# Performance work log

Hardware: AMD Instinct MI355X
Metric: run time of the kernel (lower is better)

The kernel has to match this reference:

```python
import jax, jax.numpy as jnp
import numpy as np

D_MODEL = 1024
NUM_HEADS = 16
D_FF = 4096
EPS = 1e-5


def _linear(x, w, b):
    # torch nn.Linear: y = x @ W^T + b, W is [out, in]
    return jnp.einsum('bld,od->blo', x, w) + b


def _layer_norm(x, g, b):
    mu = jnp.mean(x, axis=-1, keepdims=True)
    var = jnp.mean(jnp.square(x - mu), axis=-1, keepdims=True)
    return (x - mu) / jnp.sqrt(var + EPS) * g + b


def _mha(q, k, v, wq, bq, wk, bk, wv, bv, wo, bo, mask, num_heads):
    B, Lq, D = q.shape
    hd = D // num_heads
    Q = _linear(q, wq, bq).reshape(B, Lq, num_heads, hd).transpose(0, 2, 1, 3)
    K = _linear(k, wk, bk).reshape(B, -1, num_heads, hd).transpose(0, 2, 1, 3)
    V = _linear(v, wv, bv).reshape(B, -1, num_heads, hd).transpose(0, 2, 1, 3)
    scale = jnp.sqrt(jnp.asarray(hd, dtype=q.dtype))
    energy = jnp.einsum('bhqd,bhkd->bhqk', Q, K) / scale  # [B,H,Lq,Lk]
    energy = jnp.where(mask, energy, jnp.asarray(-1e10, dtype=q.dtype))
    attn = jax.nn.softmax(energy, axis=-1)
    x = jnp.einsum('bhqk,bhkd->bhqd', attn, V)
    x = x.transpose(0, 2, 1, 3).reshape(B, Lq, D)
    return _linear(x, wo, bo), attn


def setup_inputs() -> dict:
    key = jax.random.key(0)
    ks = iter(jax.random.split(key, 40))
    B, T, S, D, F = 4, 1024, 1024, D_MODEL, D_FF
    inp = {
        'tgt': jax.random.normal(next(ks), (B, T, D), dtype=jnp.float32),
        'enc_src': jax.random.normal(next(ks), (B, S, D), dtype=jnp.float32),
        'tgt_mask': jnp.tril(jnp.ones((1, 1, T, T), dtype=bool)),
        'src_mask': jnp.ones((1, 1, 1, S), dtype=bool),
    }
    def lin(kk, o, i):
        return jax.random.normal(kk, (o, i), dtype=jnp.float32) * 0.02
    for pfx in ('sa', 'ca'):  # self-attn and cross-attn params
        for nm in ('q', 'k', 'v', 'o'):
            inp[f'{pfx}_w{nm}'] = lin(next(ks), D, D)
            inp[f'{pfx}_b{nm}'] = jnp.zeros((D,), dtype=jnp.float32)
    inp['ff_w1'] = lin(next(ks), F, D)
    inp['ff_b1'] = jnp.zeros((F,), dtype=jnp.float32)
    inp['ff_w2'] = lin(next(ks), D, F)
    inp['ff_b2'] = jnp.zeros((D,), dtype=jnp.float32)
    for i in (1, 2, 3):
        inp[f'ln{i}_g'] = jnp.ones((D,), dtype=jnp.float32)
        inp[f'ln{i}_b'] = jnp.zeros((D,), dtype=jnp.float32)
    return inp


def reference(tgt, enc_src, tgt_mask, src_mask,
              sa_wq, sa_bq, sa_wk, sa_bk, sa_wv, sa_bv, sa_wo, sa_bo,
              ca_wq, ca_bq, ca_wk, ca_bk, ca_wv, ca_bv, ca_wo, ca_bo,
              ff_w1, ff_b1, ff_w2, ff_b2,
              ln1_g, ln1_b, ln2_g, ln2_b, ln3_g, ln3_b):
    # dropout in eval mode (identity)
    _t, _ = _mha(tgt, tgt, tgt, sa_wq, sa_bq, sa_wk, sa_bk, sa_wv, sa_bv,
                 sa_wo, sa_bo, tgt_mask, NUM_HEADS)
    tgt = _layer_norm(tgt + _t, ln1_g, ln1_b)
    _t, attention = _mha(tgt, enc_src, enc_src, ca_wq, ca_bq, ca_wk, ca_bk,
                         ca_wv, ca_bv, ca_wo, ca_bo, src_mask, NUM_HEADS)
    tgt = _layer_norm(tgt + _t, ln2_g, ln2_b)
    _t = _linear(jax.nn.relu(_linear(tgt, ff_w1, ff_b1)), ff_w2, ff_b2)
    tgt = _layer_norm(tgt + _t, ln3_g, ln3_b)
    return tgt, attention
```

## Files before the change

### kernel.cpp

```cpp
#include <hip/hip_runtime.h>
#include <hip/hip_bf16.h>

#define BBATCH 4
#define TT 1024
#define SS 1024
#define DD 1024
#define HH 16
#define HD 64
#define FFD 4096
#define MM (BBATCH*TT)

using f32x4  = __attribute__((ext_vector_type(4))) float;
using s16x8  = __attribute__((ext_vector_type(8))) short;
using bf16x8 = __attribute__((ext_vector_type(8))) __bf16;

__device__ __forceinline__ unsigned short f2b(float f) {
  union { float f; unsigned int u; } x{f};
  unsigned int r = x.u + 0x7FFFu + ((x.u >> 16) & 1u);
  return (unsigned short)(r >> 16);
}

__device__ __forceinline__ float b2f(unsigned short u) {
  union { unsigned int i; float f; } x; x.i = (unsigned int)u << 16; return x.f;
}

__device__ __forceinline__ void gload16(const void* g, void* l) {
  __builtin_amdgcn_global_load_lds(
      (const __attribute__((address_space(1))) void*)g,
      (__attribute__((address_space(3))) void*)l, 16, 0, 0);
}

__device__ __forceinline__ f32x4 mfma_bf16(s16x8 a, s16x8 b, f32x4 c) {
  return __builtin_amdgcn_mfma_f32_16x16x32_bf16(
      __builtin_bit_cast(bf16x8, a), __builtin_bit_cast(bf16x8, b), c, 0, 0, 0);
}

template <int JT, int NSUB>
__device__ __forceinline__ void gemm_core(
    const unsigned short* __restrict__ Ab, int lda,
    const unsigned short* __restrict__ Bb, int ldb,
    int K, unsigned short* As, unsigned short* Bs, f32x4 (&acc)[4][JT])
{
  const int tid = threadIdx.x, wave = tid >> 6, lane = tid & 63;
  const int r0 = tid >> 2, c0 = (tid & 3) * 8;
  const int wrow = (wave >> 1) * 64, wcol = (wave & 1) * 16 * JT;
  const int q = lane >> 4, rl = lane & 15;
  const s16x8* Av = (const s16x8*)As;
  const s16x8* Bv = (const s16x8*)Bs;

  for (int k0 = 0; k0 < K; k0 += 32 * NSUB) {
#pragma unroll
    for (int s = 0; s < NSUB; s++) {
      int kk = k0 + s * 32;
      gload16(Ab + (size_t)r0 * lda + kk + c0, As + s * 4096 + wave * 512);
      gload16(Ab + (size_t)(r0 + 64) * lda + kk + c0, As + s * 4096 + wave * 512 + 2048);
      gload16(Bb + (size_t)r0 * ldb + kk + c0, Bs + s * (JT * 1024) + wave * 512);
      if (JT == 4)
        gload16(Bb + (size_t)(r0 + 64) * ldb + kk + c0, Bs + s * (JT * 1024) + wave * 512 + 2048);
    }
    __syncthreads();
#pragma unroll
    for (int s = 0; s < NSUB; s++) {
      s16x8 af[4], bfr[JT];
#pragma unroll
      for (int t = 0; t < 4; t++) af[t] = Av[s * 512 + (wrow + t * 16 + rl) * 4 + q];
#pragma unroll
      for (int t = 0; t < JT; t++) bfr[t] = Bv[s * (JT * 128) + (wcol + t * 16 + rl) * 4 + q];
#pragma unroll
      for (int i = 0; i < 4; i++)
#pragma unroll
        for (int j = 0; j < JT; j++)
          acc[i][j] = mfma_bf16(af[i], bfr[j], acc[i][j]);
    }
    __syncthreads();
  }
}

template <int EPI, int JT, int NSUB>
__global__ __launch_bounds__(256) void gemm_bt(
    const unsigned short* __restrict__ A, int lda,
    const unsigned short* __restrict__ B, int ldb,
    const float* __restrict__ bias, const float* __restrict__ res,
    float* __restrict__ Cf, unsigned short* __restrict__ Cb, int ldc, int K)
{
  __shared__ __align__(16) unsigned short As[NSUB * 128 * 32];
  __shared__ __align__(16) unsigned short Bs[NSUB * JT * 1024];
  const int bm = blockIdx.y, bn = blockIdx.x;
  const int lane = threadIdx.x & 63, wave = threadIdx.x >> 6;
  const int wrow = (wave >> 1) * 64, wcol = (wave & 1) * 16 * JT;
  const int q = lane >> 4, rl = lane & 15;

  f32x4 acc[4][JT];
  f32x4 z = {0.f, 0.f, 0.f, 0.f};
#pragma unroll
  for (int i = 0; i < 4; i++)
#pragma unroll
    for (int j = 0; j < JT; j++) acc[i][j] = z;

  gemm_core<JT, NSUB>(A + (size_t)bm * 128 * lda, lda,
                      B + (size_t)bn * (32 * JT) * ldb, ldb, K, As, Bs, acc);

#pragma unroll
  for (int i = 0; i < 4; i++) {
    int gm0 = bm * 128 + wrow + i * 16 + q * 4;
#pragma unroll
    for (int j = 0; j < JT; j++) {
      int gn = bn * (32 * JT) + wcol + j * 16 + rl;
      float bv = bias[gn];
#pragma unroll
      for (int r = 0; r < 4; r++) {
        size_t off = (size_t)(gm0 + r) * ldc + gn;
        float v = acc[i][j][r];
        if constexpr (EPI == 0) Cb[off] = f2b(v + bv);
        else if constexpr (EPI == 2) Cf[off] = v + bv + res[off];
        else Cb[off] = f2b(fmaxf(v + bv, 0.f));
      }
    }
  }
}

__global__ __launch_bounds__(256) void gemm_qkvkv(
    const unsigned short* __restrict__ Xb, const unsigned short* __restrict__ Eb,
    const unsigned short* __restrict__ Wqkv1, const unsigned short* __restrict__ Wkv2,
    const float* __restrict__ bqkv, const float* __restrict__ bkv,
    unsigned short* __restrict__ QKVb, unsigned short* __restrict__ KVb,
    unsigned short* __restrict__ Vt1, unsigned short* __restrict__ Vt2)
{
  __shared__ __align__(16) unsigned short lds[16384];
  unsigned short* As = lds;
  unsigned short* Bs = lds + 8192;
  const int tid = threadIdx.x;
  const int bm = blockIdx.y, bn = blockIdx.x;
  const int lane = tid & 63, wave = tid >> 6;
  const int wrow = (wave >> 1) * 64, wcol = (wave & 1) * 64;
  const int q = lane >> 4, rl = lane & 15;

  const unsigned short *A, *Bw;
  const float* bias;
  unsigned short *C, *Vt;
  int ldc, vbn;
  bool isV;
  if (bn < 24) {
    A = Xb; Bw = Wqkv1 + (size_t)bn * 128 * 1024; bias = bqkv + bn * 128;
    C = QKVb + bn * 128; ldc = 3072;
    isV = (bn >= 16); Vt = Vt1; vbn = bn - 16;
  } else {
    int b2 = bn - 24;
    A = Eb; Bw = Wkv2 + (size_t)b2 * 128 * 1024; bias = bkv + b2 * 128;
    C = KVb + b2 * 128; ldc = 2048;
    isV = (b2 >= 8); Vt = Vt2; vbn = b2 - 8;
  }

  f32x4 acc[4][4];
  f32x4 z = {0.f, 0.f, 0.f, 0.f};
#pragma unroll
  for (int i = 0; i < 4; i++)
#pragma unroll
    for (int j = 0; j < 4; j++) acc[i][j] = z;

  gemm_core<4, 2>(A + (size_t)bm * 128 * 1024, 1024, Bw, 1024, 1024, As, Bs, acc);

  if (!isV) {
#pragma unroll
    for (int i = 0; i < 4; i++) {
      int lr0 = wrow + i * 16 + q * 4;
#pragma unroll
      for (int j = 0; j < 4; j++) {
        int lc = wcol + j * 16 + rl;
        float bv = bias[lc];
#pragma unroll
        for (int r = 0; r < 4; r++)
          C[(size_t)(bm * 128 + lr0 + r) * ldc + lc] = f2b(acc[i][j][r] + bv);
      }
    }
  } else {
#pragma unroll
    for (int i = 0; i < 4; i++) {
      int lr0 = wrow + i * 16 + q * 4;
#pragma unroll
      for (int j = 0; j < 4; j++) {
        int lc = wcol + j * 16 + rl;
        float bv = bias[lc];
        int base = lc * 128, sw = (lc & 7) << 2;
#pragma unroll
        for (int r = 0; r < 4; r++)
          lds[base + ((lr0 + r) ^ sw)] = f2b(acc[i][j][r] + bv);
      }
    }
    __syncthreads();
    const int b = bm >> 3, s0 = (bm & 7) * 128;
#pragma unroll
    for (int it = 0; it < 16; it++) {
      int idx = it * 256 + tid;
      int lc = idx >> 5, qa = idx & 31;
      ushort4 v4 = *(const ushort4*)&lds[lc * 128 + ((qa ^ (lc & 7)) << 2)];
      int h = vbn * 2 + (lc >> 6), d = lc & 63;
      *(ushort4*)&Vt[(((size_t)b * 16 + h) * 64 + d) * 1024 + s0 + qa * 4] = v4;
    }
  }
}

__device__ __forceinline__ void sblock_qk(
    const unsigned short* Qs, const unsigned short* Ks,
    int wrow, int wcol, int q, int rl, f32x4 (&acc)[4][4])
{
  const s16x8* Qv = (const s16x8*)Qs;
  const s16x8* Kv = (const s16x8*)Ks;
  f32x4 z = {0.f, 0.f, 0.f, 0.f};
#pragma unroll
  for (int i = 0; i < 4; i++)
#pragma unroll
    for (int j = 0; j < 4; j++) acc[i][j] = z;
#pragma unroll
  for (int kq = 0; kq < 2; kq++) {
    s16x8 af[4], bf[4];
#pragma unroll
    for (int t = 0; t < 4; t++) af[t] = Qv[kq * 512 + (wrow + t * 16 + rl) * 4 + q];
#pragma unroll
    for (int t = 0; t < 4; t++) bf[t] = Kv[kq * 512 + (wcol + t * 16 + rl) * 4 + q];
#pragma unroll
    for (int i = 0; i < 4; i++)
#pragma unroll
      for (int j = 0; j < 4; j++)
        acc[i][j] = mfma_bf16(af[i], bf[j], acc[i][j]);
  }
}

__device__ __forceinline__ void store_ps_swz(
    unsigned short* Ps, const f32x4 (&acc)[4][4], int wrow, int wcol, int q, int rl)
{
#pragma unroll
  for (int i = 0; i < 4; i++)
#pragma unroll
    for (int j = 0; j < 4; j++) {
      int col = wcol + j * 16 + rl;
      int ks = col >> 5, cc = col & 31;
#pragma unroll
      for (int r = 0; r < 4; r++) {
        int row = wrow + i * 16 + q * 4 + r;
        int unit = (row * 4 + (cc >> 3)) ^ ((row >> 1) & 3);
        Ps[ks * 4096 + unit * 8 + (cc & 7)] = f2b(acc[i][j][r]);
      }
    }
}

__device__ __forceinline__ void pv_swz(
    const unsigned short* Ps, const unsigned short* Vs,
    int wrow, int wc2, int q, int rl, f32x4 (&oacc)[4][2])
{
  const s16x8* Pv = (const s16x8*)Ps;
  const s16x8* Vv = (const s16x8*)Vs;
#pragma unroll
  for (int ks = 0; ks < 4; ks++) {
    s16x8 af[4], bf[2];
#pragma unroll
    for (int t = 0; t < 4; t++) {
      int row = wrow + t * 16 + rl;
      af[t] = Pv[ks * 512 + ((row * 4 + q) ^ ((row >> 1) & 3))];
    }
#pragma unroll
    for (int t = 0; t < 2; t++) bf[t] = Vv[ks * 256 + (wc2 + t * 16 + rl) * 4 + q];
#pragma unroll
    for (int i = 0; i < 4; i++)
#pragma unroll
      for (int jt = 0; jt < 2; jt++)
        oacc[i][jt] = mfma_bf16(af[i], bf[jt], oacc[i][jt]);
  }
}

__global__ __launch_bounds__(256, 2) void flash_sa(
    const unsigned short* __restrict__ Qg, int ldq,
    const unsigned short* __restrict__ Kg, int ldk,
    const unsigned short* __restrict__ Vt,
    unsigned short* __restrict__ Og)
{
  __shared__ __align__(16) unsigned short Qs[2 * 128 * 32];
  __shared__ __align__(16) unsigned short Ks[2 * 128 * 32];
  __shared__ __align__(16) unsigned short Vs[4 * 64 * 32];
  __shared__ __align__(16) unsigned short Ps[4 * 128 * 32];

  const int tid = threadIdx.x, wave = tid >> 6, lane = tid & 63;
  const int q = lane >> 4, rl = lane & 15;
  const int bh = blockIdx.y, b = bh >> 4, h = bh & 15;
  const int bm = (bh & 32) ? (7 - blockIdx.x) : blockIdx.x;
  const int wrow = (wave >> 1) * 64, wcol = (wave & 1) * 64;
  const int wc2 = (wave & 1) * 32;
  const int r0 = tid >> 2, c0 = (tid & 3) * 8;

  const unsigned short* Qbase = Qg + ((size_t)b * TT + bm * 128) * ldq + h * HD;
  const unsigned short* Kbase = Kg + (size_t)b * SS * ldk + h * HD;
  const unsigned short* Vbase = Vt + ((size_t)bh << 16);

#pragma unroll
  for (int kq = 0; kq < 2; kq++) {
    gload16(Qbase + (size_t)r0 * ldq + kq * 32 + c0, Qs + kq * 4096 + wave * 512);
    gload16(Qbase + (size_t)(r0 + 64) * ldq + kq * 32 + c0, Qs + kq * 4096 + wave * 512 + 2048);
  }
  const int nch = bm + 1;

  float l_run[4][4];
  f32x4 oacc[4][2];
  f32x4 z = {0.f, 0.f, 0.f, 0.f};
#pragma unroll
  for (int i = 0; i < 4; i++) {
    oacc[i][0] = z; oacc[i][1] = z;
#pragma unroll
    for (int r = 0; r < 4; r++) l_run[i][r] = 0.f;
  }

  for (int c = 0; c < nch; c++) {
    const unsigned short* src = Kbase + (size_t)c * 128 * ldk;
#pragma unroll
    for (int kq = 0; kq < 2; kq++) {
      gload16(src + (size_t)r0 * ldk + kq * 32 + c0, Ks + kq * 4096 + wave * 512);
      gload16(src + (size_t)(r0 + 64) * ldk + kq * 32 + c0, Ks + kq * 4096 + wave * 512 + 2048);
    }
#pragma unroll
    for (int ks = 0; ks < 4; ks++)
      gload16(Vbase + (size_t)r0 * SS + c * 128 + ks * 32 + c0, Vs + ks * 2048 + wave * 512);
    __syncthreads();

    f32x4 acc[4][4];
    sblock_qk(Qs, Ks, wrow, wcol, q, rl, acc);
#pragma unroll
    for (int i = 0; i < 4; i++)
#pragma unroll
      for (int r = 0; r < 4; r++) {
#pragma unroll
        for (int j = 0; j < 4; j++) {
          float v = acc[i][j][r] * 0.125f;
          bool msk = (c == bm) && (wcol + j * 16 + rl) > (wrow + i * 16 + q * 4 + r);
          acc[i][j][r] = msk ? 0.f : __expf(v);
        }
        float s = acc[i][0][r] + acc[i][1][r] + acc[i][2][r] + acc[i][3][r];
#pragma unroll
        for (int off = 1; off < 16; off <<= 1) s += __shfl_xor(s, off);
        l_run[i][r] += s;
      }
    store_ps_swz(Ps, acc, wrow, wcol, q, rl);
    __syncthreads();
    pv_swz(Ps, Vs, wrow, wc2, q, rl, oacc);
    __syncthreads();
  }

  float* red = (float*)Ps;
  if (rl == 0) {
#pragma unroll
    for (int i = 0; i < 4; i++)
#pragma unroll
      for (int r = 0; r < 4; r++)
        red[(wave & 1) * 128 + wrow + i * 16 + q * 4 + r] = l_run[i][r];
  }
  __syncthreads();

#pragma unroll
  for (int i = 0; i < 4; i++) {
#pragma unroll
    for (int r = 0; r < 4; r++) {
      int row = wrow + i * 16 + q * 4 + r;
      float inv = 1.0f / (red[row] + red[128 + row]);
      int grow = bm * 128 + row;
#pragma unroll
      for (int jt = 0; jt < 2; jt++) {
        int col = h * HD + wc2 + jt * 16 + rl;
        Og[((size_t)b * TT + grow) * DD + col] = f2b(oacc[i][jt][r] * inv);
      }
    }
  }
}

__global__ __launch_bounds__(256, 2) void flash_ca(
    const unsigned short* __restrict__ Qg, int ldq,
    const unsigned short* __restrict__ Kg, int ldk,
    const unsigned short* __restrict__ Vt,
    float* __restrict__ Pout,
    unsigned short* __restrict__ Og)
{
  __shared__ __align__(16) unsigned short Qs[2 * 128 * 32];
  __shared__ __align__(16) unsigned short Ks[2 * 128 * 32];
  __shared__ __align__(16) unsigned short Vs[4 * 64 * 32];
  __shared__ __align__(16) unsigned short Ps[4 * 128 * 32];

  const int tid = threadIdx.x, wave = tid >> 6, lane = tid & 63;
  const int q = lane >> 4, rl = lane & 15;
  const int bm = blockIdx.x, bh = blockIdx.y, b = bh >> 4, h = bh & 15;
  const int wrow = (wave >> 1) * 64, wcol = (wave & 1) * 64;
  const int wc2 = (wave & 1) * 32;
  const int r0 = tid >> 2, c0 = (tid & 3) * 8;

  const unsigned short* Qbase = Qg + ((size_t)b * TT + bm * 128) * ldq + h * HD;
  const unsigned short* Kbase = Kg + (size_t)b * SS * ldk + h * HD;
  const unsigned short* Vbase = Vt + ((size_t)bh << 16);

#pragma unroll
  for (int kq = 0; kq < 2; kq++) {
    gload16(Qbase + (size_t)r0 * ldq + kq * 32 + c0, Qs + kq * 4096 + wave * 512);
    gload16(Qbase + (size_t)(r0 + 64) * ldq + kq * 32 + c0, Qs + kq * 4096 + wave * 512 + 2048);
  }

  float l_run[4][4];
#pragma unroll
  for (int i = 0; i < 4; i++)
#pragma unroll
    for (int r = 0; r < 4; r++) l_run[i][r] = 0.f;

  for (int c = 0; c < 8; c++) {
    const unsigned short* src = Kbase + (size_t)c * 128 * ldk;
#pragma unroll
    for (int kq = 0; kq < 2; kq++) {
      gload16(src + (size_t)r0 * ldk + kq * 32 + c0, Ks + kq * 4096 + wave * 512);
      gload16(src + (size_t)(r0 + 64) * ldk + kq * 32 + c0, Ks + kq * 4096 + wave * 512 + 2048);
    }
    __syncthreads();
    f32x4 acc[4][4];
    sblock_qk(Qs, Ks, wrow, wcol, q, rl, acc);
#pragma unroll
    for (int i = 0; i < 4; i++)
#pragma unroll
      for (int r = 0; r < 4; r++) {
        float s = __expf(acc[i][0][r] * 0.125f) + __expf(acc[i][1][r] * 0.125f) +
                  __expf(acc[i][2][r] * 0.125f) + __expf(acc[i][3][r] * 0.125f);
#pragma unroll
        for (int off = 1; off < 16; off <<= 1) s += __shfl_xor(s, off);
        l_run[i][r] += s;
      }
    __syncthreads();
  }
  float* red = (float*)Ps;
  if (rl == 0) {
#pragma unroll
    for (int i = 0; i < 4; i++)
#pragma unroll
      for (int r = 0; r < 4; r++)
        red[(wave & 1) * 128 + wrow + i * 16 + q * 4 + r] = l_run[i][r];
  }
  __syncthreads();
  float invl[4][4];
#pragma unroll
  for (int i = 0; i < 4; i++)
#pragma unroll
    for (int r = 0; r < 4; r++) {
      int row = wrow + i * 16 + q * 4 + r;
      invl[i][r] = 1.0f / (red[row] + red[128 + row]);
    }

  f32x4 oacc[4][2];
  f32x4 z = {0.f, 0.f, 0.f, 0.f};
#pragma unroll
  for (int i = 0; i < 4; i++) { oacc[i][0] = z; oacc[i][1] = z; }

  for (int c = 0; c < 8; c++) {
    const unsigned short* src = Kbase + (size_t)c * 128 * ldk;
#pragma unroll
    for (int kq = 0; kq < 2; kq++) {
      gload16(src + (size_t)r0 * ldk + kq * 32 + c0, Ks + kq * 4096 + wave * 512);
      gload16(src + (size_t)(r0 + 64) * ldk + kq * 32 + c0, Ks + kq * 4096 + wave * 512 + 2048);
    }
#pragma unroll
    for (int ks = 0; ks < 4; ks++)
      gload16(Vbase + (size_t)r0 * SS + c * 128 + ks * 32 + c0, Vs + ks * 2048 + wave * 512);
    __syncthreads();
    f32x4 acc[4][4];
    sblock_qk(Qs, Ks, wrow, wcol, q, rl, acc);
#pragma unroll
    for (int i = 0; i < 4; i++)
#pragma unroll
      for (int j = 0; j < 4; j++)
#pragma unroll
        for (int r = 0; r < 4; r++)
          acc[i][j][r] = __expf(acc[i][j][r] * 0.125f) * invl[i][r];
    store_ps_swz(Ps, acc, wrow, wcol, q, rl);
    __syncthreads();
#pragma unroll
    for (int it = 0; it < 8; it++) {
      int idx = it * 256 + tid;
      int ks = idx >> 9, rw = (idx >> 2) & 127, u = idx & 3;
      s16x8 pv = ((const s16x8*)Ps)[ks * 512 + ((rw * 4 + u) ^ ((rw >> 1) & 3))];
      float4 lo = make_float4(b2f((unsigned short)pv[0]), b2f((unsigned short)pv[1]),
                              b2f((unsigned short)pv[2]), b2f((unsigned short)pv[3]));
      float4 hi = make_float4(b2f((unsigned short)pv[4]), b2f((unsigned short)pv[5]),
                              b2f((unsigned short)pv[6]), b2f((unsigned short)pv[7]));
      float* dst = Pout + ((size_t)bh << 20) + ((size_t)(bm * 128 + rw) << 10) +
                   c * 128 + ks * 32 + u * 8;
      ((float4*)dst)[0] = lo;
      ((float4*)dst)[1] = hi;
    }
    pv_swz(Ps, Vs, wrow, wc2, q, rl, oacc);
    __syncthreads();
  }

#pragma unroll
  for (int i = 0; i < 4; i++)
#pragma unroll
    for (int jt = 0; jt < 2; jt++)
#pragma unroll
      for (int r = 0; r < 4; r++) {
        int row = bm * 128 + wrow + i * 16 + q * 4 + r;
        int col = h * HD + wc2 + jt * 16 + rl;
        Og[((size_t)b * TT + row) * DD + col] = f2b(oacc[i][jt][r]);
      }
}

__global__ __launch_bounds__(256) void ln_k(
    const float* __restrict__ src, const float* __restrict__ g,
    const float* __restrict__ b, float* __restrict__ dstf,
    unsigned short* __restrict__ dstb)
{
  __shared__ float sh[10];
  const size_t row = blockIdx.x;
  const int tid = threadIdx.x;
  float4 v = ((const float4*)(src + (row << 10)))[tid];
  float s = v.x + v.y + v.z + v.w;
  float ss = v.x * v.x + v.y * v.y + v.z * v.z + v.w * v.w;
  for (int o = 32; o; o >>= 1) { s += __shfl_down(s, o); ss += __shfl_down(ss, o); }
  if ((tid & 63) == 0) { sh[tid >> 6] = s; sh[4 + (tid >> 6)] = ss; }
  __syncthreads();
  if (tid == 0) {
    sh[8] = sh[0] + sh[1] + sh[2] + sh[3];
    sh[9] = sh[4] + sh[5] + sh[6] + sh[7];
  }
  __syncthreads();
  const float mean = sh[8] * (1.0f / DD);
  const float var = sh[9] * (1.0f / DD) - mean * mean;
  const float inv = rsqrtf(var + 1e-5f);
  float4 gv = ((const float4*)g)[tid];
  float4 bv = ((const float4*)b)[tid];
  float4 y;
  y.x = (v.x - mean) * inv * gv.x + bv.x;
  y.y = (v.y - mean) * inv * gv.y + bv.y;
  y.z = (v.z - mean) * inv * gv.z + bv.z;
  y.w = (v.w - mean) * inv * gv.w + bv.w;
  if (dstf) ((float4*)(dstf + (row << 10)))[tid] = y;
  if (dstb) {
    ushort4 o = make_ushort4(f2b(y.x), f2b(y.y), f2b(y.z), f2b(y.w));
    ((ushort4*)(dstb + (row << 10)))[tid] = o;
  }
}

struct CvtArgs {
  const float* src[12];
  unsigned short* dst[12];
};

__global__ __launch_bounds__(256) void cvt_all(CvtArgs a) {
  constexpr int st[13] = {0,       1048576, 2097152, 2359296, 2621440,
                          2883584, 3145728, 3407872, 3670016, 3932160,
                          4194304, 5242880, 6291456};
  int i = blockIdx.x * 256 + threadIdx.x;
  int s = 0;
#pragma unroll
  for (int k = 1; k < 12; k++) s += (i >= st[k]) ? 1 : 0;
  int j = i - st[s];
  float4 v = ((const float4*)a.src[s])[j];
  ushort4 o = make_ushort4(f2b(v.x), f2b(v.y), f2b(v.z), f2b(v.w));
  ((ushort4*)a.dst[s])[j] = o;
}

__global__ __launch_bounds__(256) void bias_pack(
    const float* __restrict__ bq, const float* __restrict__ bk, const float* __restrict__ bv,
    const float* __restrict__ bk2, const float* __restrict__ bv2,
    float* __restrict__ bqkv, float* __restrict__ bkv)
{
  int i = blockIdx.x * 256 + threadIdx.x;
  if (i < 1024) bqkv[i] = bq[i];
  else if (i < 2048) bqkv[i] = bk[i - 1024];
  else if (i < 3072) bqkv[i] = bv[i - 2048];
  else if (i < 4096) bkv[i - 3072] = bk2[i - 3072];
  else if (i < 5120) bkv[i - 3072] = bv2[i - 4096 + 1024];
}


extern "C" void kernel_launch(void* const* d_in, const int* in_sizes, int n_in,
                              void* d_out, int out_size, void* d_ws, size_t ws_size,
                              hipStream_t stream)
{
  const float* tgt = (const float*)d_in[0];
  const float* enc = (const float*)d_in[1];
  const float* sa_wq = (const float*)d_in[4];  const float* sa_bq = (const float*)d_in[5];
  const float* sa_wk = (const float*)d_in[6];  const float* sa_bk = (const float*)d_in[7];
  const float* sa_wv = (const float*)d_in[8];  const float* sa_bv = (const float*)d_in[9];
  const float* sa_wo = (const float*)d_in[10]; const float* sa_bo = (const float*)d_in[11];
  const float* ca_wq = (const float*)d_in[12]; const float* ca_bq = (const float*)d_in[13];
  const float* ca_wk = (const float*)d_in[14]; const float* ca_bk = (const float*)d_in[15];
  const float* ca_wv = (const float*)d_in[16]; const float* ca_bv = (const float*)d_in[17];
  const float* ca_wo = (const float*)d_in[18]; const float* ca_bo = (const float*)d_in[19];
  const float* ff_w1 = (const float*)d_in[20]; const float* ff_b1 = (const float*)d_in[21];
  const float* ff_w2 = (const float*)d_in[22]; const float* ff_b2 = (const float*)d_in[23];
  const float* ln1_g = (const float*)d_in[24]; const float* ln1_b = (const float*)d_in[25];
  const float* ln2_g = (const float*)d_in[26]; const float* ln2_b = (const float*)d_in[27];
  const float* ln3_g = (const float*)d_in[28]; const float* ln3_b = (const float*)d_in[29];

  float* out_tgt = (float*)d_out;
  float* out_attn = (float*)d_out + (size_t)MM * DD;

  char* w = (char*)d_ws;
  size_t off = 0;
  auto alloc = [&](size_t bytes) { void* p = w + off; off += (bytes + 255) & ~(size_t)255; return p; };
  unsigned short* Xb   = (unsigned short*)alloc((size_t)MM * DD * 2);
  unsigned short* Eb   = (unsigned short*)alloc((size_t)MM * DD * 2);
  unsigned short* Wq1  = (unsigned short*)alloc((size_t)DD * DD * 2);
  unsigned short* Wk1  = (unsigned short*)alloc((size_t)DD * DD * 2);
  unsigned short* Wv1  = (unsigned short*)alloc((size_t)DD * DD * 2);
  unsigned short* Wo1  = (unsigned short*)alloc((size_t)DD * DD * 2);
  unsigned short* Wq2  = (unsigned short*)alloc((size_t)DD * DD * 2);
  unsigned short* Wk2  = (unsigned short*)alloc((size_t)DD * DD * 2);
  unsigned short* Wv2  = (unsigned short*)alloc((size_t)DD * DD * 2);
  unsigned short* Wo2  = (unsigned short*)alloc((size_t)DD * DD * 2);
  unsigned short* Wf1  = (unsigned short*)alloc((size_t)FFD * DD * 2);
  unsigned short* Wf2  = (unsigned short*)alloc((size_t)DD * FFD * 2);
  unsigned short* QKVb = (unsigned short*)alloc((size_t)MM * 3 * DD * 2);
  unsigned short* KVb  = (unsigned short*)alloc((size_t)MM * 2 * DD * 2);
  unsigned short* Qca  = (unsigned short*)alloc((size_t)MM * DD * 2);
  unsigned short* Vt1  = (unsigned short*)alloc((size_t)MM * DD * 2);
  unsigned short* Vt2  = (unsigned short*)alloc((size_t)MM * DD * 2);
  unsigned short* Ob   = (unsigned short*)alloc((size_t)MM * DD * 2);
  float*          res1 = (float*)alloc((size_t)MM * DD * 4);
  unsigned short* t1b  = (unsigned short*)alloc((size_t)MM * DD * 2);
  float*          res2 = (float*)alloc((size_t)MM * DD * 4);
  unsigned short* t2b  = (unsigned short*)alloc((size_t)MM * DD * 2);
  unsigned short* Fb   = (unsigned short*)alloc((size_t)MM * FFD * 2);
  float*          bqkv = (float*)alloc(3072 * 4);
  float*          bkv  = (float*)alloc(2048 * 4);

  CvtArgs ca;
  ca.src[0] = tgt;   ca.dst[0] = Xb;
  ca.src[1] = enc;   ca.dst[1] = Eb;
  ca.src[2] = sa_wq; ca.dst[2] = Wq1;
  ca.src[3] = sa_wk; ca.dst[3] = Wk1;
  ca.src[4] = sa_wv; ca.dst[4] = Wv1;
  ca.src[5] = sa_wo; ca.dst[5] = Wo1;
  ca.src[6] = ca_wq; ca.dst[6] = Wq2;
  ca.src[7] = ca_wk; ca.dst[7] = Wk2;
  ca.src[8] = ca_wv; ca.dst[8] = Wv2;
  ca.src[9] = ca_wo; ca.dst[9] = Wo2;
  ca.src[10] = ff_w1; ca.dst[10] = Wf1;
  ca.src[11] = ff_w2; ca.dst[11] = Wf2;

  bias_pack<<<20, 256, 0, stream>>>(sa_bq, sa_bk, sa_bv, ca_bk, ca_bv, bqkv, bkv);
  cvt_all<<<24576, 256, 0, stream>>>(ca);

  const dim3 gPRJ(40, 32);
  const dim3 gN64(16, 32);
  const dim3 gFF1(32, 32);
  const dim3 gFl(8, 64);

  gemm_qkvkv<<<gPRJ, 256, 0, stream>>>(Xb, Eb, Wq1, Wk2, bqkv, bkv,
                                       QKVb, KVb, Vt1, Vt2);

  flash_sa<<<gFl, 256, 0, stream>>>(QKVb, 3 * DD, QKVb + DD, 3 * DD, Vt1, Ob);
  gemm_bt<2, 2, 4><<<gN64, 256, 0, stream>>>(Ob, DD, Wo1, DD, sa_bo, tgt, res1, nullptr, DD, DD);
  ln_k<<<MM, 256, 0, stream>>>(res1, ln1_g, ln1_b, res1, t1b);

  gemm_bt<0, 2, 4><<<gN64, 256, 0, stream>>>(t1b, DD, Wq2, DD, ca_bq, nullptr, nullptr, Qca, DD, DD);
  flash_ca<<<gFl, 256, 0, stream>>>(Qca, DD, KVb, 2 * DD, Vt2, out_attn, Ob);
  gemm_bt<2, 2, 4><<<gN64, 256, 0, stream>>>(Ob, DD, Wo2, DD, ca_bo, res1, res2, nullptr, DD, DD);
  ln_k<<<MM, 256, 0, stream>>>(res2, ln2_g, ln2_b, res2, t2b);

  gemm_bt<3, 4, 2><<<gFF1, 256, 0, stream>>>(t2b, DD, Wf1, DD, ff_b1, nullptr, nullptr, Fb, FFD, DD);
  gemm_bt<2, 2, 4><<<gN64, 256, 0, stream>>>(Fb, FFD, Wf2, FFD, ff_b2, res2, res1, nullptr, DD, FFD);
  ln_k<<<MM, 256, 0, stream>>>(res1, ln3_g, ln3_b, out_tgt, nullptr);
}
```

Measured before the change: 781.4 us.

## Double-buffer K tiles, load V fragments to registers, XCD-swizzle GEMM grids

The flash attention kernels now double-buffer the K tile in LDS, prefetching the next chunk after the loop-top barrier, and drop one barrier per iteration. V fragments are read straight from global memory into registers, which removes the V staging buffer in LDS. The GEMM kernels remap block indices so neighbouring tiles are spread round-robin across the 8 XCDs, aiming for better L2 reuse. The trade-offs are more register pressure from holding V fragments, uncoalesced 16-byte V reads, and a swizzle that assumes the grid size is divisible by 8.

```diff
diff --git a/kernel.cpp b/kernel.cpp
--- a/kernel.cpp
+++ b/kernel.cpp
@@ -35,6 +35,13 @@
       __builtin_bit_cast(bf16x8, a), __builtin_bit_cast(bf16x8, b), c, 0, 0, 0);
 }
 
+__device__ __forceinline__ void xcd_swz(int gx, int& bn, int& bm) {
+  int flat = blockIdx.y * gx + blockIdx.x;
+  int nwg = gx * gridDim.y;
+  int swz = (flat & 7) * (nwg >> 3) + (flat >> 3);
+  bn = swz % gx; bm = swz / gx;
+}
+
 template <int JT, int NSUB>
 __device__ __forceinline__ void gemm_core(
     const unsigned short* __restrict__ Ab, int lda,
@@ -85,7 +92,8 @@
 {
   __shared__ __align__(16) unsigned short As[NSUB * 128 * 32];
   __shared__ __align__(16) unsigned short Bs[NSUB * JT * 1024];
-  const int bm = blockIdx.y, bn = blockIdx.x;
+  int bm, bn;
+  xcd_swz(gridDim.x, bn, bm);
   const int lane = threadIdx.x & 63, wave = threadIdx.x >> 6;
   const int wrow = (wave >> 1) * 64, wcol = (wave & 1) * 16 * JT;
   const int q = lane >> 4, rl = lane & 15;
@@ -130,7 +138,8 @@
   unsigned short* As = lds;
   unsigned short* Bs = lds + 8192;
   const int tid = threadIdx.x;
-  const int bm = blockIdx.y, bn = blockIdx.x;
+  int bm, bn;
+  xcd_swz(gridDim.x, bn, bm);
   const int lane = tid & 63, wave = tid >> 6;
   const int wrow = (wave >> 1) * 64, wcol = (wave & 1) * 64;
   const int q = lane >> 4, rl = lane & 15;
@@ -200,6 +209,17 @@
   }
 }
 
+__device__ __forceinline__ void stage_k(
+    const unsigned short* src, int ldk, unsigned short* Kbuf,
+    int r0, int c0, int wave)
+{
+#pragma unroll
+  for (int kq = 0; kq < 2; kq++) {
+    gload16(src + (size_t)r0 * ldk + kq * 32 + c0, Kbuf + kq * 4096 + wave * 512);
+    gload16(src + (size_t)(r0 + 64) * ldk + kq * 32 + c0, Kbuf + kq * 4096 + wave * 512 + 2048);
+  }
+}
+
 __device__ __forceinline__ void sblock_qk(
     const unsigned short* Qs, const unsigned short* Ks,
     int wrow, int wcol, int q, int rl, f32x4 (&acc)[4][4])
@@ -224,6 +244,17 @@
       for (int j = 0; j < 4; j++)
         acc[i][j] = mfma_bf16(af[i], bf[j], acc[i][j]);
   }
+}
+
+__device__ __forceinline__ void load_vf(
+    const unsigned short* Vbase, int c, int wc2, int q, int rl, s16x8 (&vf)[4][2])
+{
+#pragma unroll
+  for (int ks = 0; ks < 4; ks++)
+#pragma unroll
+    for (int t = 0; t < 2; t++)
+      vf[ks][t] = *(const s16x8*)(Vbase + (size_t)(wc2 + t * 16 + rl) * SS +
+                                  c * 128 + ks * 32 + q * 8);
 }
 
 __device__ __forceinline__ void store_ps_swz(
@@ -245,26 +276,23 @@
 }
 
 __device__ __forceinline__ void pv_swz(
-    const unsigned short* Ps, const unsigned short* Vs,
-    int wrow, int wc2, int q, int rl, f32x4 (&oacc)[4][2])
+    const unsigned short* Ps, const s16x8 (&vf)[4][2],
+    int wrow, int q, int rl, f32x4 (&oacc)[4][2])
 {
   const s16x8* Pv = (const s16x8*)Ps;
-  const s16x8* Vv = (const s16x8*)Vs;
 #pragma unroll
   for (int ks = 0; ks < 4; ks++) {
-    s16x8 af[4], bf[2];
+    s16x8 af[4];
 #pragma unroll
     for (int t = 0; t < 4; t++) {
       int row = wrow + t * 16 + rl;
       af[t] = Pv[ks * 512 + ((row * 4 + q) ^ ((row >> 1) & 3))];
     }
 #pragma unroll
-    for (int t = 0; t < 2; t++) bf[t] = Vv[ks * 256 + (wc2 + t * 16 + rl) * 4 + q];
-#pragma unroll
     for (int i = 0; i < 4; i++)
 #pragma unroll
       for (int jt = 0; jt < 2; jt++)
-        oacc[i][jt] = mfma_bf16(af[i], bf[jt], oacc[i][jt]);
+        oacc[i][jt] = mfma_bf16(af[i], vf[ks][jt], oacc[i][jt]);
   }
 }
 
@@ -275,8 +303,7 @@
     unsigned short* __restrict__ Og)
 {
   __shared__ __align__(16) unsigned short Qs[2 * 128 * 32];
-  __shared__ __align__(16) unsigned short Ks[2 * 128 * 32];
-  __shared__ __align__(16) unsigned short Vs[4 * 64 * 32];
+  __shared__ __align__(16) unsigned short Ks[2][2 * 128 * 32];
   __shared__ __align__(16) unsigned short Ps[4 * 128 * 32];
 
   const int tid = threadIdx.x, wave = tid >> 6, lane = tid & 63;
@@ -296,6 +323,7 @@
     gload16(Qbase + (size_t)r0 * ldq + kq * 32 + c0, Qs + kq * 4096 + wave * 512);
     gload16(Qbase + (size_t)(r0 + 64) * ldq + kq * 32 + c0, Qs + kq * 4096 + wave * 512 + 2048);
   }
+  stage_k(Kbase, ldk, Ks[0], r0, c0, wave);
   const int nch = bm + 1;
 
   float l_run[4][4];
@@ -309,19 +337,13 @@
   }
 
   for (int c = 0; c < nch; c++) {
-    const unsigned short* src = Kbase + (size_t)c * 128 * ldk;
-#pragma unroll
-    for (int kq = 0; kq < 2; kq++) {
-      gload16(src + (size_t)r0 * ldk + kq * 32 + c0, Ks + kq * 4096 + wave * 512);
-      gload16(src + (size_t)(r0 + 64) * ldk + kq * 32 + c0, Ks + kq * 4096 + wave * 512 + 2048);
-    }
-#pragma unroll
-    for (int ks = 0; ks < 4; ks++)
-      gload16(Vbase + (size_t)r0 * SS + c * 128 + ks * 32 + c0, Vs + ks * 2048 + wave * 512);
-    __syncthreads();
-
+    __syncthreads();
+    if (c + 1 < nch)
+      stage_k(Kbase + (size_t)(c + 1) * 128 * ldk, ldk, Ks[(c + 1) & 1], r0, c0, wave);
+    s16x8 vf[4][2];
+    load_vf(Vbase, c, wc2, q, rl, vf);
     f32x4 acc[4][4];
-    sblock_qk(Qs, Ks, wrow, wcol, q, rl, acc);
+    sblock_qk(Qs, Ks[c & 1], wrow, wcol, q, rl, acc);
 #pragma unroll
     for (int i = 0; i < 4; i++)
 #pragma unroll
@@ -339,9 +361,9 @@
       }
     store_ps_swz(Ps, acc, wrow, wcol, q, rl);
     __syncthreads();
-    pv_swz(Ps, Vs, wrow, wc2, q, rl, oacc);
-    __syncthreads();
-  }
+    pv_swz(Ps, vf, wrow, q, rl, oacc);
+  }
+  __syncthreads();
 
   float* red = (float*)Ps;
   if (rl == 0) {
@@ -377,8 +399,7 @@
     unsigned short* __restrict__ Og)
 {
   __shared__ __align__(16) unsigned short Qs[2 * 128 * 32];
-  __shared__ __align__(16) unsigned short Ks[2 * 128 * 32];
-  __shared__ __align__(16) unsigned short Vs[4 * 64 * 32];
+  __shared__ __align__(16) unsigned short Ks[2][2 * 128 * 32];
   __shared__ __align__(16) unsigned short Ps[4 * 128 * 32];
 
   const int tid = threadIdx.x, wave = tid >> 6, lane = tid & 63;
@@ -397,6 +418,7 @@
     gload16(Qbase + (size_t)r0 * ldq + kq * 32 + c0, Qs + kq * 4096 + wave * 512);
     gload16(Qbase + (size_t)(r0 + 64) * ldq + kq * 32 + c0, Qs + kq * 4096 + wave * 512 + 2048);
   }
+  stage_k(Kbase, ldk, Ks[0], r0, c0, wave);
 
   float l_run[4][4];
 #pragma unroll
@@ -405,15 +427,11 @@
     for (int r = 0; r < 4; r++) l_run[i][r] = 0.f;
 
   for (int c = 0; c < 8; c++) {
-    const unsigned short* src = Kbase + (size_t)c * 128 * ldk;
-#pragma unroll
-    for (int kq = 0; kq < 2; kq++) {
-      gload16(src + (size_t)r0 * ldk + kq * 32 + c0, Ks + kq * 4096 + wave * 512);
-      gload16(src + (size_t)(r0 + 64) * ldk + kq * 32 + c0, Ks + kq * 4096 + wave * 512 + 2048);
-    }
-    __syncthreads();
+    __syncthreads();
+    if (c < 7)
+      stage_k(Kbase + (size_t)(c + 1) * 128 * ldk, ldk, Ks[(c + 1) & 1], r0, c0, wave);
     f32x4 acc[4][4];
-    sblock_qk(Qs, Ks, wrow, wcol, q, rl, acc);
+    sblock_qk(Qs, Ks[c & 1], wrow, wcol, q, rl, acc);
 #pragma unroll
     for (int i = 0; i < 4; i++)
 #pragma unroll
@@ -424,7 +442,6 @@
         for (int off = 1; off < 16; off <<= 1) s += __shfl_xor(s, off);
         l_run[i][r] += s;
       }
-    __syncthreads();
   }
   float* red = (float*)Ps;
   if (rl == 0) {
@@ -448,20 +465,16 @@
   f32x4 z = {0.f, 0.f, 0.f, 0.f};
 #pragma unroll
   for (int i = 0; i < 4; i++) { oacc[i][0] = z; oacc[i][1] = z; }
+  stage_k(Kbase, ldk, Ks[0], r0, c0, wave);
 
   for (int c = 0; c < 8; c++) {
-    const unsigned short* src = Kbase + (size_t)c * 128 * ldk;
-#pragma unroll
-    for (int kq = 0; kq < 2; kq++) {
-      gload16(src + (size_t)r0 * ldk + kq * 32 + c0, Ks + kq * 4096 + wave * 512);
-      gload16(src + (size_t)(r0 + 64) * ldk + kq * 32 + c0, Ks + kq * 4096 + wave * 512 + 2048);
-    }
-#pragma unroll
-    for (int ks = 0; ks < 4; ks++)
-      gload16(Vbase + (size_t)r0 * SS + c * 128 + ks * 32 + c0, Vs + ks * 2048 + wave * 512);
-    __syncthreads();
+    __syncthreads();
+    if (c < 7)
+      stage_k(Kbase + (size_t)(c + 1) * 128 * ldk, ldk, Ks[(c + 1) & 1], r0, c0, wave);
+    s16x8 vf[4][2];
+    load_vf(Vbase, c, wc2, q, rl, vf);
     f32x4 acc[4][4];
-    sblock_qk(Qs, Ks, wrow, wcol, q, rl, acc);
+    sblock_qk(Qs, Ks[c & 1], wrow, wcol, q, rl, acc);
 #pragma unroll
     for (int i = 0; i < 4; i++)
 #pragma unroll
@@ -485,8 +498,7 @@
       ((float4*)dst)[0] = lo;
       ((float4*)dst)[1] = hi;
     }
-    pv_swz(Ps, Vs, wrow, wc2, q, rl, oacc);
-    __syncthreads();
+    pv_swz(Ps, vf, wrow, q, rl, oacc);
   }
 
 #pragma unroll
```

After: 768.8 us. No clear change (-1.6%).
